# Optimization experiments

Hardware: AMD Instinct MI355X
Metric: run time of the kernel (lower is better)

## Reference

```python
import jax, jax.numpy as jnp
import numpy as np

B = 4096          # batch_size
NUM_SWARM = 100
NUM_SCOUTS = 28
NUM_HIVES = 64
NUM_AGENTS = NUM_SWARM + NUM_SCOUTS          # 128
NUM_ENTITIES = NUM_AGENTS + NUM_HIVES        # 192
VOCAB = 32
D_DISC, K_DISC, T_DISC = 100.0, 30.0, 0.7


def setup_inputs() -> dict:
    key = jax.random.key(0)
    k1, k2, k3, k4, k5 = jax.random.split(key, 5)
    return {
        "movements": jax.random.normal(k1, (B, NUM_ENTITIES, 2), dtype=jnp.float32),
        "utterances": jax.random.normal(k2, (B, NUM_AGENTS, VOCAB), dtype=jnp.float32),
        "votes": jax.random.normal(k3, (B, NUM_AGENTS, NUM_HIVES), dtype=jnp.float32),
        "hive_values": jax.random.uniform(k4, (B, NUM_HIVES, 1), dtype=jnp.float32),
        "locations": jax.random.uniform(k5, (B, NUM_ENTITIES, 2), dtype=jnp.float32),
    }


def reference(movements, utterances, votes, hive_values, locations):
    # --- movement cost: sum over all entities of L2 norm of movement ---
    movement_cost = jnp.sqrt(jnp.sum(movements * movements, axis=-1)).sum()

    # --- per-agent vote selection: argmax over hives ---
    agent_vote = jnp.argmax(votes, axis=2)                       # [B, A] int

    # --- value(): gather hive values by vote index, sum per batch ---
    # (vectorized form of the original per-batch Python loop)
    hv = hive_values[:, :, 0]                                    # [B, H]
    value = jnp.take_along_axis(hv, agent_vote, axis=1).sum(axis=1)  # [B]

    # --- max_freq(): per-batch histogram of votes via scatter-add ---
    counts = jnp.zeros((B, NUM_HIVES), dtype=jnp.float32)
    counts = counts.at[jnp.arange(B)[:, None], agent_vote].add(1.0)  # [B, H]
    max_freq = counts.max(axis=1) / NUM_AGENTS                   # [B]

    # --- discounted vote cost ---
    discount = D_DISC * (1.0 - jax.nn.sigmoid(K_DISC * (max_freq - T_DISC)))
    vote_cost = -(value / discount).sum()

    return (vote_cost + movement_cost, max_freq)
```

## Files before the change

kernel.cpp:

```cpp
#include <hip/hip_runtime.h>
#include <math.h>

#define NUM_AGENTS   128
#define NUM_HIVES    64
#define NUM_ENTITIES 192

__global__ __launch_bounds__(256) void bee_kernel(
    const float* __restrict__ movements,
    const float* __restrict__ votes,
    const float* __restrict__ hive_values,
    float* __restrict__ ws_partial,
    float* __restrict__ out)
{
    const int b    = blockIdx.x;
    const int tid  = threadIdx.x;
    const int lane = tid & 63;
    const int wave = tid >> 6;

    __shared__ float hv[NUM_HIVES];
    __shared__ int   counts[NUM_HIVES];
    __shared__ float mc_s[4];
    __shared__ float vs_s[4];

    if (tid < NUM_HIVES) {
        hv[tid]     = hive_values[(size_t)b * NUM_HIVES + tid];
        counts[tid] = 0;
    }
    __syncthreads();

    float mc = 0.0f;
    if (tid < NUM_ENTITIES) {
        float2 m = ((const float2*)movements)[(size_t)b * NUM_ENTITIES + tid];
        mc = sqrtf(m.x * m.x + m.y * m.y);
    }

    const int grp = lane >> 4;
    const int gl  = lane & 15;
    const float4* vbase = (const float4*)(votes + (size_t)b * NUM_AGENTS * NUM_HIVES);

    float vsum = 0.0f;
    #pragma unroll
    for (int iter = 0; iter < 8; ++iter) {
        const int a = iter * 16 + wave * 4 + grp;
        float4 v = vbase[a * 16 + gl];

        float bestv = v.x; int besti = gl * 4;
        if (v.y > bestv) { bestv = v.y; besti = gl * 4 + 1; }
        if (v.z > bestv) { bestv = v.z; besti = gl * 4 + 2; }
        if (v.w > bestv) { bestv = v.w; besti = gl * 4 + 3; }

        #pragma unroll
        for (int off = 1; off < 16; off <<= 1) {
            float ov = __shfl_xor(bestv, off, 64);
            int   oi = __shfl_xor(besti, off, 64);
            if (ov > bestv || (ov == bestv && oi < besti)) { bestv = ov; besti = oi; }
        }

        if (gl == 0) {
            atomicAdd(&counts[besti], 1);
            vsum += hv[besti];
        }
    }

    #pragma unroll
    for (int off = 32; off > 0; off >>= 1) {
        mc   += __shfl_down(mc,   off, 64);
        vsum += __shfl_down(vsum, off, 64);
    }
    if (lane == 0) { mc_s[wave] = mc; vs_s[wave] = vsum; }
    __syncthreads();

    if (wave == 0) {
        int c = counts[lane];
        #pragma unroll
        for (int off = 32; off > 0; off >>= 1) {
            int oc = __shfl_down(c, off, 64);
            c = c > oc ? c : oc;
        }
        if (lane == 0) {
            float mc_t = mc_s[0] + mc_s[1] + mc_s[2] + mc_s[3];
            float vs_t = vs_s[0] + vs_s[1] + vs_s[2] + vs_s[3];
            float mf = (float)c / (float)NUM_AGENTS;
            out[1 + b] = mf;
            float discount = 100.0f / (1.0f + expf(30.0f * (mf - 0.7f)));
            ws_partial[b] = mc_t - vs_t / discount;
        }
    }
}

__global__ __launch_bounds__(256) void reduce_kernel(
    const float* __restrict__ ws_partial, float* __restrict__ out, int B)
{
    const int tid  = threadIdx.x;
    const int lane = tid & 63;
    const int wave = tid >> 6;
    __shared__ float p_s[4];

    float s = 0.0f;
    const float4* w4 = (const float4*)ws_partial;
    for (int i = tid; i < B / 4; i += 256) {
        float4 v = w4[i];
        s += (v.x + v.y) + (v.z + v.w);
    }
    #pragma unroll
    for (int off = 32; off > 0; off >>= 1) s += __shfl_down(s, off, 64);
    if (lane == 0) p_s[wave] = s;
    __syncthreads();
    if (tid == 0) out[0] = p_s[0] + p_s[1] + p_s[2] + p_s[3];
}

extern "C" void kernel_launch(void* const* d_in, const int* in_sizes, int n_in,
                              void* d_out, int out_size, void* d_ws, size_t ws_size,
                              hipStream_t stream) {
    const float* movements   = (const float*)d_in[0];
    const float* votes       = (const float*)d_in[2];
    const float* hive_values = (const float*)d_in[3];
    float* out = (float*)d_out;
    float* ws_partial = (float*)d_ws;

    const int B = in_sizes[3] / NUM_HIVES;

    bee_kernel<<<B, 256, 0, stream>>>(movements, votes, hive_values, ws_partial, out);
    reduce_kernel<<<1, 256, 0, stream>>>(ws_partial, out, B);
}
```

Before: 234.7 us.

## Map one wavefront per batch row with per-lane agent argmax

Each 256-thread block now handles four batch rows, one per wavefront, instead of one row per block. Each lane scans two full 64-wide vote rows serially, so the 16-lane shuffle argmax reductions and the shared hive-value table go away. Hive values are kept in registers and fetched with lane shuffles. The final reductions are fused into a single xor-shuffle loop. Each lane now reads its own contiguous row, so a single load instruction spans many cache lines. That gives up coalescing in exchange for more memory-level parallelism and fewer cross-lane operations.

```diff
diff --git a/kernel.cpp b/kernel.cpp
--- a/kernel.cpp
+++ b/kernel.cpp
@@ -4,86 +4,79 @@
 #define NUM_AGENTS   128
 #define NUM_HIVES    64
 #define NUM_ENTITIES 192
+#define BPB 4
 
 __global__ __launch_bounds__(256) void bee_kernel(
     const float* __restrict__ movements,
     const float* __restrict__ votes,
     const float* __restrict__ hive_values,
     float* __restrict__ ws_partial,
-    float* __restrict__ out)
+    float* __restrict__ out,
+    int B)
 {
-    const int b    = blockIdx.x;
     const int tid  = threadIdx.x;
     const int lane = tid & 63;
     const int wave = tid >> 6;
+    const int b    = blockIdx.x * BPB + wave;
 
-    __shared__ float hv[NUM_HIVES];
-    __shared__ int   counts[NUM_HIVES];
-    __shared__ float mc_s[4];
-    __shared__ float vs_s[4];
+    __shared__ int counts[BPB][NUM_HIVES];
 
-    if (tid < NUM_HIVES) {
-        hv[tid]     = hive_values[(size_t)b * NUM_HIVES + tid];
-        counts[tid] = 0;
+    counts[wave][lane] = 0;
+
+    float hv_reg = 0.0f, mc = 0.0f, bv0 = -INFINITY, bv1 = -INFINITY;
+    int bi0 = 0, bi1 = 0;
+
+    if (b < B) {
+        hv_reg = hive_values[(size_t)b * NUM_HIVES + lane];
+
+        const float2* mv = (const float2*)movements + (size_t)b * NUM_ENTITIES;
+        float2 m0 = mv[lane];
+        float2 m1 = mv[lane + 64];
+        float2 m2 = mv[lane + 128];
+        mc = sqrtf(m0.x*m0.x + m0.y*m0.y)
+           + sqrtf(m1.x*m1.x + m1.y*m1.y)
+           + sqrtf(m2.x*m2.x + m2.y*m2.y);
+
+        const float4* r0 = (const float4*)(votes + ((size_t)b * NUM_AGENTS + lane)      * NUM_HIVES);
+        const float4* r1 = (const float4*)(votes + ((size_t)b * NUM_AGENTS + lane + 64) * NUM_HIVES);
+
+        #pragma unroll
+        for (int k = 0; k < 16; ++k) {
+            float4 v0 = r0[k];
+            float4 v1 = r1[k];
+            if (v0.x > bv0) { bv0 = v0.x; bi0 = k*4 + 0; }
+            if (v0.y > bv0) { bv0 = v0.y; bi0 = k*4 + 1; }
+            if (v0.z > bv0) { bv0 = v0.z; bi0 = k*4 + 2; }
+            if (v0.w > bv0) { bv0 = v0.w; bi0 = k*4 + 3; }
+            if (v1.x > bv1) { bv1 = v1.x; bi1 = k*4 + 0; }
+            if (v1.y > bv1) { bv1 = v1.y; bi1 = k*4 + 1; }
+            if (v1.z > bv1) { bv1 = v1.z; bi1 = k*4 + 2; }
+            if (v1.w > bv1) { bv1 = v1.w; bi1 = k*4 + 3; }
+        }
     }
     __syncthreads();
 
-    float mc = 0.0f;
-    if (tid < NUM_ENTITIES) {
-        float2 m = ((const float2*)movements)[(size_t)b * NUM_ENTITIES + tid];
-        mc = sqrtf(m.x * m.x + m.y * m.y);
+    float vsum = 0.0f;
+    if (b < B) {
+        atomicAdd(&counts[wave][bi0], 1);
+        atomicAdd(&counts[wave][bi1], 1);
+        vsum = __shfl(hv_reg, bi0, 64) + __shfl(hv_reg, bi1, 64);
     }
-
-    const int grp = lane >> 4;
-    const int gl  = lane & 15;
-    const float4* vbase = (const float4*)(votes + (size_t)b * NUM_AGENTS * NUM_HIVES);
-
-    float vsum = 0.0f;
-    #pragma unroll
-    for (int iter = 0; iter < 8; ++iter) {
-        const int a = iter * 16 + wave * 4 + grp;
-        float4 v = vbase[a * 16 + gl];
-
-        float bestv = v.x; int besti = gl * 4;
-        if (v.y > bestv) { bestv = v.y; besti = gl * 4 + 1; }
-        if (v.z > bestv) { bestv = v.z; besti = gl * 4 + 2; }
-        if (v.w > bestv) { bestv = v.w; besti = gl * 4 + 3; }
-
-        #pragma unroll
-        for (int off = 1; off < 16; off <<= 1) {
-            float ov = __shfl_xor(bestv, off, 64);
-            int   oi = __shfl_xor(besti, off, 64);
-            if (ov > bestv || (ov == bestv && oi < besti)) { bestv = ov; besti = oi; }
-        }
-
-        if (gl == 0) {
-            atomicAdd(&counts[besti], 1);
-            vsum += hv[besti];
-        }
-    }
-
-    #pragma unroll
-    for (int off = 32; off > 0; off >>= 1) {
-        mc   += __shfl_down(mc,   off, 64);
-        vsum += __shfl_down(vsum, off, 64);
-    }
-    if (lane == 0) { mc_s[wave] = mc; vs_s[wave] = vsum; }
     __syncthreads();
 
-    if (wave == 0) {
-        int c = counts[lane];
+    if (b < B) {
+        int c = counts[wave][lane];
         #pragma unroll
         for (int off = 32; off > 0; off >>= 1) {
-            int oc = __shfl_down(c, off, 64);
-            c = c > oc ? c : oc;
+            c     = max(c, __shfl_xor(c, off, 64));
+            mc   += __shfl_xor(mc,   off, 64);
+            vsum += __shfl_xor(vsum, off, 64);
         }
         if (lane == 0) {
-            float mc_t = mc_s[0] + mc_s[1] + mc_s[2] + mc_s[3];
-            float vs_t = vs_s[0] + vs_s[1] + vs_s[2] + vs_s[3];
-            float mf = (float)c / (float)NUM_AGENTS;
+            float mf = (float)c * (1.0f / (float)NUM_AGENTS);
             out[1 + b] = mf;
             float discount = 100.0f / (1.0f + expf(30.0f * (mf - 0.7f)));
-            ws_partial[b] = mc_t - vs_t / discount;
+            ws_partial[b] = mc - vsum / discount;
         }
     }
 }
@@ -120,6 +113,7 @@
 
     const int B = in_sizes[3] / NUM_HIVES;
 
-    bee_kernel<<<B, 256, 0, stream>>>(movements, votes, hive_values, ws_partial, out);
+    const int grid = (B + BPB - 1) / BPB;
+    bee_kernel<<<grid, 256, 0, stream>>>(movements, votes, hive_values, ws_partial, out, B);
     reduce_kernel<<<1, 256, 0, stream>>>(ws_partial, out, B);
 }
```

New measurement: 251.7 us. +7.2%, slower.
